# Kernel optimization log

Hardware: AMD Instinct MI355X
Metric: run time of the kernel (lower is better)

## Reference

```python
import jax, jax.numpy as jnp
import numpy as np

D_MODEL = 1024
NUM_HEADS = 16
D_K = D_MODEL // NUM_HEADS
B, S = 2, 2048


def setup_inputs() -> dict:
    key = jax.random.key(0)
    ks = jax.random.split(key, 11)
    sc = 1.0 / np.sqrt(D_MODEL)
    return {
        "query": jax.random.normal(ks[0], (B, S, D_MODEL), jnp.float32),
        "key": jax.random.normal(ks[1], (B, S, D_MODEL), jnp.float32),
        "value": jax.random.normal(ks[2], (B, S, D_MODEL), jnp.float32),
        "Wq": jax.random.normal(ks[3], (D_MODEL, D_MODEL), jnp.float32) * sc,
        "bq": jnp.zeros((D_MODEL,), jnp.float32),
        "Wk": jax.random.normal(ks[4], (D_MODEL, D_MODEL), jnp.float32) * sc,
        "bk": jnp.zeros((D_MODEL,), jnp.float32),
        "Wv": jax.random.normal(ks[5], (D_MODEL, D_MODEL), jnp.float32) * sc,
        "bv": jnp.zeros((D_MODEL,), jnp.float32),
        "Wo": jax.random.normal(ks[6], (D_MODEL, D_MODEL), jnp.float32) * sc,
        "bo": jnp.zeros((D_MODEL,), jnp.float32),
    }


def reference(query, key, value, Wq, bq, Wk, bk, Wv, bv, Wo, bo):
    b, sq, _ = query.shape
    # projections -> [B, H, S, d_k]
    def split_heads(x):
        return x.reshape(b, -1, NUM_HEADS, D_K).transpose(0, 2, 1, 3)

    q = split_heads(query @ Wq + bq)
    k = split_heads(key @ Wk + bk)
    v = split_heads(value @ Wv + bv)

    scores = jnp.einsum("bhqd,bhkd->bhqk", q, k) / np.sqrt(D_K).astype(np.float32)
    probs = jax.nn.softmax(scores, axis=-1)  # dropout p=0 (eval) -> identity
    attn = jnp.einsum("bhqk,bhkd->bhqd", probs, v)
    attn = attn.transpose(0, 2, 1, 3).reshape(b, sq, D_MODEL)
    out = attn @ Wo + bo
    return out, probs
```

## Files before the change

kernel.cpp:

```cpp
#include <hip/hip_runtime.h>


typedef __bf16 bf16x8 __attribute__((ext_vector_type(8)));
typedef float f32x4 __attribute__((ext_vector_type(4)));

typedef const unsigned int __attribute__((address_space(1))) as1c_uint;
typedef unsigned int __attribute__((address_space(3))) as3_uint;

#define S_LEN 2048
#define DM 1024
#define NH 16
#define DK 64
#define BATCH 2
#define M_ROWS 4096
#define KE 0.18033688f

__device__ __forceinline__ unsigned short f2bfu(float f) {
  union { __bf16 b; unsigned short u; } cv;
  cv.b = (__bf16)f;
  return cv.u;
}

__device__ __forceinline__ float bfu2f(unsigned short u) {
  union { float f; unsigned int i; } c;
  c.i = ((unsigned int)u) << 16;
  return c.f;
}

__device__ __forceinline__ void gload_lds16(const void* g, void* l) {
  __builtin_amdgcn_global_load_lds((as1c_uint*)g, (as3_uint*)l, 16, 0, 0);
}

__global__ __launch_bounds__(256) void cvt3_kernel(
    const float* __restrict__ q, const float* __restrict__ k,
    const float* __restrict__ v, unsigned short* __restrict__ oq,
    unsigned short* __restrict__ ok_, unsigned short* __restrict__ ov) {
  const float* in = blockIdx.z == 0 ? q : (blockIdx.z == 1 ? k : v);
  unsigned short* out = blockIdx.z == 0 ? oq : (blockIdx.z == 1 ? ok_ : ov);
  size_t i = (size_t)blockIdx.x * 256 + threadIdx.x;
  float4 f = ((const float4*)in)[i];
  ushort4 u;
  u.x = f2bfu(f.x); u.y = f2bfu(f.y); u.z = f2bfu(f.z); u.w = f2bfu(f.w);
  ((ushort4*)out)[i] = u;
}

__global__ __launch_bounds__(256) void wtrans_kernel(
    const float* __restrict__ w0, const float* __restrict__ w1,
    const float* __restrict__ w2, const float* __restrict__ w3,
    unsigned short* __restrict__ o0, unsigned short* __restrict__ o1,
    unsigned short* __restrict__ o2, unsigned short* __restrict__ o3) {
  const float* W = blockIdx.z == 0 ? w0 : (blockIdx.z == 1 ? w1 : (blockIdx.z == 2 ? w2 : w3));
  unsigned short* WT = blockIdx.z == 0 ? o0 : (blockIdx.z == 1 ? o1 : (blockIdx.z == 2 ? o2 : o3));
  __shared__ float tile[32][33];
  int tx = threadIdx.x & 31, ty = threadIdx.x >> 5;
  int bx = blockIdx.x * 32, by = blockIdx.y * 32;
#pragma unroll
  for (int i = 0; i < 32; i += 8)
    tile[ty + i][tx] = W[(size_t)(by + ty + i) * DM + bx + tx];
  __syncthreads();
#pragma unroll
  for (int i = 0; i < 32; i += 8)
    WT[(size_t)(bx + ty + i) * DM + by + tx] = f2bfu(tile[tx][ty + i]);
}

template <int EPI>
__device__ __forceinline__ void gemm_core(const unsigned short* __restrict__ A,
                                          const unsigned short* __restrict__ BT,
                                          const float* __restrict__ bias,
                                          void* __restrict__ C) {
  __shared__ __attribute__((aligned(16))) unsigned short As[128 * 32];
  __shared__ __attribute__((aligned(16))) unsigned short Bs[128 * 32];
  const int tid = threadIdx.x;
  const int w = tid >> 6, l = tid & 63;
  const int wr = w >> 1, wc = w & 1;
  const int fr = l & 15, fq = l >> 4;
  const int m0 = blockIdx.y * 128, n0 = blockIdx.x * 128;
  const int srow = l >> 2;
  const int sk8 = (l & 3) * 8;
  f32x4 acc[4][4] = {};

  for (int k0 = 0; k0 < DM; k0 += 32) {
#pragma unroll
    for (int c = 0; c < 2; c++) {
      int r = c * 64 + w * 16;
      gload_lds16(A + (size_t)(m0 + r + srow) * DM + k0 + sk8, As + (size_t)r * 32);
      gload_lds16(BT + (size_t)(n0 + r + srow) * DM + k0 + sk8, Bs + (size_t)r * 32);
    }
    __syncthreads();
    bf16x8 af[4], bfv[4];
#pragma unroll
    for (int m = 0; m < 4; m++)
      af[m] = *(const bf16x8*)(As + (size_t)(wr * 64 + m * 16 + fr) * 32 + fq * 8);
#pragma unroll
    for (int n = 0; n < 4; n++)
      bfv[n] = *(const bf16x8*)(Bs + (size_t)(wc * 64 + n * 16 + fr) * 32 + fq * 8);
#pragma unroll
    for (int m = 0; m < 4; m++)
#pragma unroll
      for (int n = 0; n < 4; n++)
        acc[m][n] = __builtin_amdgcn_mfma_f32_16x16x32_bf16(af[m], bfv[n], acc[m][n], 0, 0, 0);
    __syncthreads();
  }

#pragma unroll
  for (int m = 0; m < 4; m++) {
#pragma unroll
    for (int n = 0; n < 4; n++) {
      const int col = n0 + wc * 64 + n * 16 + fr;
      const float bv = bias[col];
#pragma unroll
      for (int j = 0; j < 4; j++) {
        const int row = m0 + wr * 64 + m * 16 + fq * 4 + j;
        const float v = acc[m][n][j] + bv;
        if (EPI == 0) {
          ((float*)C)[(size_t)row * DM + col] = v;
        } else {
          const int b = row >> 11, s = row & (S_LEN - 1);
          const int h = col >> 6, d = col & (DK - 1);
          ((unsigned short*)C)[(((size_t)b * NH + h) * S_LEN + s) * DK + d] = f2bfu(v);
        }
      }
    }
  }
}

__global__ __launch_bounds__(256) void gemm_qkv_kernel(
    const unsigned short* __restrict__ xq, const unsigned short* __restrict__ xk,
    const unsigned short* __restrict__ xv, const unsigned short* __restrict__ wq,
    const unsigned short* __restrict__ wk, const unsigned short* __restrict__ wv,
    const float* __restrict__ bq, const float* __restrict__ bk,
    const float* __restrict__ bv, unsigned short* __restrict__ oq,
    unsigned short* __restrict__ okk, unsigned short* __restrict__ ov) {
  const int z = blockIdx.z;
  const unsigned short* A = z == 0 ? xq : (z == 1 ? xk : xv);
  const unsigned short* BT = z == 0 ? wq : (z == 1 ? wk : wv);
  const float* bias = z == 0 ? bq : (z == 1 ? bk : bv);
  unsigned short* C = z == 0 ? oq : (z == 1 ? okk : ov);
  gemm_core<1>(A, BT, bias, C);
}

__global__ __launch_bounds__(256) void gemm_out_kernel(
    const unsigned short* __restrict__ A, const unsigned short* __restrict__ BT,
    const float* __restrict__ bias, float* __restrict__ C) {
  gemm_core<0>(A, BT, bias, C);
}

__global__ __launch_bounds__(256) void vtrans_kernel(
    const unsigned short* __restrict__ V, unsigned short* __restrict__ VT) {
  __shared__ __attribute__((aligned(16))) unsigned short t[64][72];
  const int bh = blockIdx.y, s0 = blockIdx.x * 64;
  const unsigned short* v = V + ((size_t)bh * S_LEN + s0) * DK;
  const int tid = threadIdx.x;
#pragma unroll
  for (int i = 0; i < 4; i++) {
    int idx = tid + 256 * i;
    int r = idx >> 4, c4 = (idx & 15) * 4;
    *(ushort4*)&t[r][c4] = *(const ushort4*)(v + (size_t)r * DK + c4);
  }
  __syncthreads();
  unsigned short* o = VT + (size_t)bh * DK * S_LEN + s0;
#pragma unroll
  for (int i = 0; i < 4; i++) {
    int idx = tid + 256 * i;
    int d = idx >> 4, s4 = (idx & 15) * 4;
    ushort4 u;
    u.x = t[s4 + 0][d]; u.y = t[s4 + 1][d];
    u.z = t[s4 + 2][d]; u.w = t[s4 + 3][d];
    *(ushort4*)(o + (size_t)d * S_LEN + s4) = u;
  }
}

__global__ __launch_bounds__(256, 4) void attn_kernel(
    const unsigned short* __restrict__ Qp, const unsigned short* __restrict__ Kp,
    const unsigned short* __restrict__ VT, float* __restrict__ probs,
    unsigned short* __restrict__ attnc) {
  const int flat = blockIdx.y * 32 + blockIdx.x;
  const int xcd = flat & 7, r = flat >> 3;
  const int bh = xcd * 4 + (r >> 5);
  const int tile = r & 31;
  const int w = threadIdx.x >> 6, l = threadIdx.x & 63;
  const int fr = l & 15, fq = l >> 4;
  const int q0 = tile * 64 + w * 16;
  const int qrow = q0 + fr;
  const unsigned short* Qh = Qp + (size_t)bh * S_LEN * DK;
  const unsigned short* Kh = Kp + (size_t)bh * S_LEN * DK;
  const unsigned short* Vh = VT + (size_t)bh * DK * S_LEN;
  float* ph = probs + (size_t)bh * S_LEN * S_LEN;

  __shared__ __attribute__((aligned(16))) unsigned short Sb[4][64 * 64];
  __shared__ __attribute__((aligned(16))) unsigned short Pfb[4][16][64];

  const int srow8 = l >> 3;
  const int sgran = ((l & 7) ^ (l >> 3)) << 3;
  const int kr7 = fr & 7;

  bf16x8 qf[2];
  qf[0] = *(const bf16x8*)(Qh + (size_t)qrow * DK + fq * 8);
  qf[1] = *(const bf16x8*)(Qh + (size_t)qrow * DK + 32 + fq * 8);

  const int NIT = S_LEN / 64;

#define STAGE_P1(itn, buf)                                                    \
  {                                                                           \
    _Pragma("unroll") for (int i = 0; i < 2; i++)                             \
        gload_lds16(Kh + (size_t)((itn) * 64 + w * 16 + i * 8 + srow8) * DK + \
                        sgran,                                                \
                    &Sb[buf][(w * 16 + i * 8) * 64]);                         \
  }

  float ps4[4] = {0.f, 0.f, 0.f, 0.f};
  STAGE_P1(0, 0);
  STAGE_P1(1, 1);
  asm volatile("s_waitcnt vmcnt(2)" : : : "memory");
  __builtin_amdgcn_s_barrier();
  for (int it = 0; it < NIT; ++it) {
    const unsigned short* kcur = &Sb[it % 3][0];
    if (it + 2 < NIT) STAGE_P1(it + 2, (it + 2) % 3);
#pragma unroll
    for (int t = 0; t < 4; t++) {
      const int rk = t * 16 + fr;
      const bf16x8 a0 = *(const bf16x8*)&kcur[rk * 64 + ((fq ^ kr7) << 3)];
      const bf16x8 a1 = *(const bf16x8*)&kcur[rk * 64 + (((fq + 4) ^ kr7) << 3)];
      f32x4 s4 = {0.f, 0.f, 0.f, 0.f};
      s4 = __builtin_amdgcn_mfma_f32_16x16x32_bf16(a0, qf[0], s4, 0, 0, 0);
      s4 = __builtin_amdgcn_mfma_f32_16x16x32_bf16(a1, qf[1], s4, 0, 0, 0);
#pragma unroll
      for (int j = 0; j < 4; j++) ps4[j] += __builtin_amdgcn_exp2f(s4[j] * KE);
    }
    if (it + 1 < NIT) {
      if (it + 2 < NIT) {
        asm volatile("s_waitcnt vmcnt(2)" : : : "memory");
      } else {
        asm volatile("s_waitcnt vmcnt(0)" : : : "memory");
      }
      __builtin_amdgcn_s_barrier();
    }
  }
#undef STAGE_P1
  float psum = (ps4[0] + ps4[1]) + (ps4[2] + ps4[3]);
  psum += __shfl_xor(psum, 16, 64);
  psum += __shfl_xor(psum, 32, 64);
  const float pinv = 1.f / psum;
  __builtin_amdgcn_s_barrier();

  f32x4 oacc[4] = {};
  const int strow = l >> 4;
  const int stc16 = l & 15;
#pragma unroll
  for (int i = 0; i < 2; i++) {
    gload_lds16(Kh + (size_t)(w * 16 + i * 8 + srow8) * DK + sgran,
                &Sb[0][(w * 16 + i * 8) * 64]);
    gload_lds16(Vh + (size_t)(w * 16 + i * 8 + srow8) * S_LEN + sgran,
                &Sb[2][(w * 16 + i * 8) * 64]);
  }
  asm volatile("s_waitcnt vmcnt(0)" : : : "memory");
  __builtin_amdgcn_s_barrier();
  for (int it = 0; it < NIT; ++it) {
    const int cur = it & 1;
    const int skb = it * 64;
    if (it + 1 < NIT) {
#pragma unroll
      for (int i = 0; i < 2; i++) {
        gload_lds16(Kh + (size_t)(skb + 64 + w * 16 + i * 8 + srow8) * DK + sgran,
                    &Sb[cur ^ 1][(w * 16 + i * 8) * 64]);
        gload_lds16(Vh + (size_t)(w * 16 + i * 8 + srow8) * S_LEN + (skb + 64) + sgran,
                    &Sb[2 + (cur ^ 1)][(w * 16 + i * 8) * 64]);
      }
    }
    if (it > 0) {
      const int skbp = skb - 64;
#pragma unroll
      for (int i = 0; i < 4; i++) {
        const int row = 4 * i + strow;
        const int g2 = ((stc16 >> 1) ^ (row & 7));
        const ushort4 pb4 = *(const ushort4*)&Pfb[w][row][g2 * 8 + (l & 1) * 4];
        f32x4 pv4;
        pv4[0] = bfu2f(pb4.x); pv4[1] = bfu2f(pb4.y);
        pv4[2] = bfu2f(pb4.z); pv4[3] = bfu2f(pb4.w);
        __builtin_nontemporal_store(
            pv4, (f32x4*)(ph + (size_t)(q0 + row) * S_LEN + skbp + stc16 * 4));
      }
    }
#pragma unroll
    for (int sub = 0; sub < 2; sub++) {
#pragma unroll
      for (int t = 0; t < 2; t++) {
        const int rk = sub * 32 + t * 16 + fr;
        const bf16x8 a0 = *(const bf16x8*)&Sb[cur][rk * 64 + ((fq ^ kr7) << 3)];
        const bf16x8 a1 = *(const bf16x8*)&Sb[cur][rk * 64 + (((fq + 4) ^ kr7) << 3)];
        f32x4 s4 = {0.f, 0.f, 0.f, 0.f};
        s4 = __builtin_amdgcn_mfma_f32_16x16x32_bf16(a0, qf[0], s4, 0, 0, 0);
        s4 = __builtin_amdgcn_mfma_f32_16x16x32_bf16(a1, qf[1], s4, 0, 0, 0);
        ushort4 pb;
#pragma unroll
        for (int j = 0; j < 4; j++)
          ((unsigned short*)&pb)[j] = f2bfu(__builtin_amdgcn_exp2f(s4[j] * KE) * pinv);
        const int g = (sub * 4 + t * 2 + (fq >> 1)) ^ kr7;
        *(ushort4*)&Pfb[w][fr][g * 8 + (fq & 1) * 4] = pb;
      }
      const int gr = (sub * 4 + fq) ^ kr7;
      const bf16x8 pa = *(const bf16x8*)&Pfb[w][fr][gr * 8];
      __builtin_amdgcn_s_setprio(1);
#pragma unroll
      for (int n = 0; n < 4; n++) {
        const bf16x8 vf =
            *(const bf16x8*)&Sb[2 + cur][(n * 16 + fr) * 64 + (((sub * 4 + fq) ^ kr7) << 3)];
        oacc[n] = __builtin_amdgcn_mfma_f32_16x16x32_bf16(pa, vf, oacc[n], 0, 0, 0);
      }
      __builtin_amdgcn_s_setprio(0);
    }
    if (it + 1 < NIT) {
      if (it == 0) {
        asm volatile("s_waitcnt vmcnt(0)" : : : "memory");
      } else {
        asm volatile("s_waitcnt vmcnt(4)" : : : "memory");
      }
      __builtin_amdgcn_s_barrier();
    }
  }
  {
    const int skbp = (NIT - 1) * 64;
#pragma unroll
    for (int i = 0; i < 4; i++) {
      const int row = 4 * i + strow;
      const int g2 = ((stc16 >> 1) ^ (row & 7));
      const ushort4 pb4 = *(const ushort4*)&Pfb[w][row][g2 * 8 + (l & 1) * 4];
      f32x4 pv4;
      pv4[0] = bfu2f(pb4.x); pv4[1] = bfu2f(pb4.y);
      pv4[2] = bfu2f(pb4.z); pv4[3] = bfu2f(pb4.w);
      __builtin_nontemporal_store(
          pv4, (f32x4*)(ph + (size_t)(q0 + row) * S_LEN + skbp + stc16 * 4));
    }
  }

  const int b = bh >> 4, h = bh & (NH - 1);
#pragma unroll
  for (int n = 0; n < 4; n++) {
#pragma unroll
    for (int j = 0; j < 4; j++) {
      const int row = q0 + fq * 4 + j, col = h * DK + n * 16 + fr;
      attnc[(size_t)((size_t)b * S_LEN + row) * DM + col] = f2bfu(oacc[n][j]);
    }
  }
}

extern "C" void kernel_launch(void* const* d_in, const int* in_sizes, int n_in,
                              void* d_out, int out_size, void* d_ws, size_t ws_size,
                              hipStream_t stream) {
  const float* query = (const float*)d_in[0];
  const float* key   = (const float*)d_in[1];
  const float* value = (const float*)d_in[2];
  const float* Wq = (const float*)d_in[3];
  const float* bq = (const float*)d_in[4];
  const float* Wk = (const float*)d_in[5];
  const float* bk = (const float*)d_in[6];
  const float* Wv = (const float*)d_in[7];
  const float* bv = (const float*)d_in[8];
  const float* Wo = (const float*)d_in[9];
  const float* bo = (const float*)d_in[10];

  char* ws = (char*)d_ws;
  const size_t XSZ = (size_t)M_ROWS * DM * 2;
  const size_t WSZ = (size_t)DM * DM * 2;
  unsigned short* xq  = (unsigned short*)(ws);
  unsigned short* xk  = (unsigned short*)(ws + XSZ);
  unsigned short* xv  = (unsigned short*)(ws + 2 * XSZ);
  unsigned short* wtq = (unsigned short*)(ws + 3 * XSZ);
  unsigned short* wtk = (unsigned short*)(ws + 3 * XSZ + WSZ);
  unsigned short* wtv = (unsigned short*)(ws + 3 * XSZ + 2 * WSZ);
  unsigned short* wto = (unsigned short*)(ws + 3 * XSZ + 3 * WSZ);
  unsigned short* qp  = (unsigned short*)(ws + 3 * XSZ + 4 * WSZ);
  unsigned short* kp  = (unsigned short*)(ws + 4 * XSZ + 4 * WSZ);
  unsigned short* vp  = (unsigned short*)(ws + 5 * XSZ + 4 * WSZ);
  unsigned short* vT    = xk;
  unsigned short* attnc = xq;

  float* out = (float*)d_out;
  float* probs = (float*)d_out + (size_t)BATCH * S_LEN * DM;

  cvt3_kernel<<<dim3(4096, 1, 3), 256, 0, stream>>>(query, key, value, xq, xk, xv);
  wtrans_kernel<<<dim3(32, 32, 4), 256, 0, stream>>>(Wq, Wk, Wv, Wo, wtq, wtk, wtv, wto);
  gemm_qkv_kernel<<<dim3(8, 32, 3), 256, 0, stream>>>(xq, xk, xv, wtq, wtk, wtv,
                                                      bq, bk, bv, qp, kp, vp);
  vtrans_kernel<<<dim3(32, 32), 256, 0, stream>>>(vp, vT);
  attn_kernel<<<dim3(32, 32), 256, 0, stream>>>(qp, kp, vT, probs, attnc);
  gemm_out_kernel<<<dim3(8, 32), 256, 0, stream>>>(attnc, wto, bo, out);
}
```

Measured before the change: 237.0 us.

## Double-buffer GEMM LDS tiles and swizzle block order for L2 reuse

```diff
diff --git a/kernel.cpp b/kernel.cpp
--- a/kernel.cpp
+++ b/kernel.cpp
@@ -68,39 +68,55 @@
                                           const unsigned short* __restrict__ BT,
                                           const float* __restrict__ bias,
                                           void* __restrict__ C) {
-  __shared__ __attribute__((aligned(16))) unsigned short As[128 * 32];
-  __shared__ __attribute__((aligned(16))) unsigned short Bs[128 * 32];
+  __shared__ __attribute__((aligned(16))) unsigned short As[2][128 * 32];
+  __shared__ __attribute__((aligned(16))) unsigned short Bs[2][128 * 32];
   const int tid = threadIdx.x;
   const int w = tid >> 6, l = tid & 63;
   const int wr = w >> 1, wc = w & 1;
   const int fr = l & 15, fq = l >> 4;
-  const int m0 = blockIdx.y * 128, n0 = blockIdx.x * 128;
+  const int bid = blockIdx.y * 8 + blockIdx.x;
+  const int swz = (bid & 7) * 32 + (bid >> 3);
+  const int n0 = (swz & 7) * 128, m0 = (swz >> 3) * 128;
   const int srow = l >> 2;
   const int sk8 = (l & 3) * 8;
   f32x4 acc[4][4] = {};
 
-  for (int k0 = 0; k0 < DM; k0 += 32) {
-#pragma unroll
-    for (int c = 0; c < 2; c++) {
-      int r = c * 64 + w * 16;
-      gload_lds16(A + (size_t)(m0 + r + srow) * DM + k0 + sk8, As + (size_t)r * 32);
-      gload_lds16(BT + (size_t)(n0 + r + srow) * DM + k0 + sk8, Bs + (size_t)r * 32);
-    }
-    __syncthreads();
+#define GSTAGE(itn, buf)                                                      \
+  {                                                                           \
+    _Pragma("unroll") for (int c = 0; c < 2; c++) {                           \
+      int rr = c * 64 + w * 16;                                               \
+      gload_lds16(A + (size_t)(m0 + rr + srow) * DM + (itn) * 32 + sk8,       \
+                  &As[buf][rr * 32]);                                         \
+      gload_lds16(BT + (size_t)(n0 + rr + srow) * DM + (itn) * 32 + sk8,      \
+                  &Bs[buf][rr * 32]);                                         \
+    }                                                                         \
+  }
+
+  const int KIT = DM / 32;
+  GSTAGE(0, 0);
+  asm volatile("s_waitcnt vmcnt(0)" : : : "memory");
+  __builtin_amdgcn_s_barrier();
+  for (int it = 0; it < KIT; ++it) {
+    const int cur = it & 1;
+    if (it + 1 < KIT) GSTAGE(it + 1, cur ^ 1);
     bf16x8 af[4], bfv[4];
 #pragma unroll
     for (int m = 0; m < 4; m++)
-      af[m] = *(const bf16x8*)(As + (size_t)(wr * 64 + m * 16 + fr) * 32 + fq * 8);
+      af[m] = *(const bf16x8*)&As[cur][(wr * 64 + m * 16 + fr) * 32 + fq * 8];
 #pragma unroll
     for (int n = 0; n < 4; n++)
-      bfv[n] = *(const bf16x8*)(Bs + (size_t)(wc * 64 + n * 16 + fr) * 32 + fq * 8);
+      bfv[n] = *(const bf16x8*)&Bs[cur][(wc * 64 + n * 16 + fr) * 32 + fq * 8];
 #pragma unroll
     for (int m = 0; m < 4; m++)
 #pragma unroll
       for (int n = 0; n < 4; n++)
         acc[m][n] = __builtin_amdgcn_mfma_f32_16x16x32_bf16(af[m], bfv[n], acc[m][n], 0, 0, 0);
-    __syncthreads();
-  }
+    if (it + 1 < KIT) {
+      asm volatile("s_waitcnt vmcnt(0)" : : : "memory");
+      __builtin_amdgcn_s_barrier();
+    }
+  }
+#undef GSTAGE
 
 #pragma unroll
   for (int m = 0; m < 4; m++) {
```

Result: faster. 231.5 us (-2.3%).
